# Optimization experiments

Hardware: AMD Instinct MI355X
Metric: run time of the kernel (lower is better)

Reference implementation:

```python
import jax, jax.numpy as jnp
import numpy as np

B, N, LAT, H, NL, NH = 1, 512, 128, 256, 3, 4
EMB = H // 4  # atom-type embedding dim = 64
DH = H // NH  # head dim = 64
LN_EPS = 1e-5


def _lin(x, w, b):
    # torch nn.Linear convention: w is (out, in)
    return x @ w.T + b


def _ln(x, s, b):
    m = jnp.mean(x, -1, keepdims=True)
    v = jnp.mean((x - m) ** 2, -1, keepdims=True)
    return (x - m) / jnp.sqrt(v + LN_EPS) * s + b


def setup_inputs() -> dict:
    key = jax.random.key(0)
    ks = iter(jax.random.split(key, 64))
    def w(shape, scale=0.02):
        return (jax.random.normal(next(ks), shape, jnp.float32) * scale).astype(jnp.float32)
    inp = dict(
        z=jax.random.normal(next(ks), (B, N, LAT), jnp.float32),
        z_global=jax.random.normal(next(ks), (B, LAT), jnp.float32),
        atom_types=jax.random.randint(next(ks), (B, N), 0, 4),
        emb=w((4, EMB), 1.0),
        ip_w1=w((H, LAT + EMB)), ip_b1=jnp.zeros(H), ip_w2=w((H, H)), ip_b2=jnp.zeros(H),
        gp_w1=w((H, LAT)), gp_b1=jnp.zeros(H), gp_w2=w((H, H)), gp_b2=jnp.zeros(H),
        tf_wqkv=w((NL, 3 * H, H)), tf_bqkv=jnp.zeros((NL, 3 * H)),
        tf_wo=w((NL, H, H)), tf_bo=jnp.zeros((NL, H)),
        tf_ln1_s=jnp.ones((NL, H)), tf_ln1_b=jnp.zeros((NL, H)),
        tf_w1=w((NL, 4 * H, H)), tf_b1=jnp.zeros((NL, 4 * H)),
        tf_w2=w((NL, H, 4 * H)), tf_b2=jnp.zeros((NL, H)),
        tf_ln2_s=jnp.ones((NL, H)), tf_ln2_b=jnp.zeros((NL, H)),
        dp_w1=w((H, 2 * H)), dp_b1=jnp.zeros(H), dp_w2=w((H, H)), dp_b2=jnp.zeros(H),
        dp_w3=w((1, H)), dp_b3=jnp.zeros(1),
        cp_w1=w((H, H)), cp_b1=jnp.zeros(H), cp_w2=w((3, H)), cp_b2=jnp.zeros(3),
    )
    return inp


def _forward(z, z_global, atom_types, emb,
             ip_w1, ip_b1, ip_w2, ip_b2,
             gp_w1, gp_b1, gp_w2, gp_b2,
             tf_wqkv, tf_bqkv, tf_wo, tf_bo, tf_ln1_s, tf_ln1_b,
             tf_w1, tf_b1, tf_w2, tf_b2, tf_ln2_s, tf_ln2_b,
             dp_w1, dp_b1, dp_w2, dp_b2, dp_w3, dp_b3,
             cp_w1, cp_b1, cp_w2, cp_b2):
    Bs, Ns = z.shape[0], z.shape[1]
    atom_feats = emb[atom_types]                      # (B,N,EMB)
    z_input = jnp.concatenate([z, atom_feats], -1)    # (B,N,LAT+EMB)
    h = _lin(jax.nn.silu(_lin(z_input, ip_w1, ip_b1)), ip_w2, ip_b2)
    g = _lin(jax.nn.silu(_lin(z_global, gp_w1, gp_b1)), gp_w2, gp_b2)
    h = h + g[:, None, :]
    # post-norm TransformerEncoder (relu FFN, eval mode -> no dropout)
    scale = 1.0 / np.sqrt(DH)
    for l in range(NL):
        qkv = _lin(h, tf_wqkv[l], tf_bqkv[l])
        q, k, v = jnp.split(qkv, 3, -1)
        q = q.reshape(Bs, Ns, NH, DH)
        k = k.reshape(Bs, Ns, NH, DH)
        v = v.reshape(Bs, Ns, NH, DH)
        att = jax.nn.softmax(jnp.einsum('bqhd,bkhd->bhqk', q, k) * scale, -1)
        o = jnp.einsum('bhqk,bkhd->bqhd', att, v).reshape(Bs, Ns, H)
        h = _ln(h + _lin(o, tf_wo[l], tf_bo[l]), tf_ln1_s[l], tf_ln1_b[l])
        ff = _lin(jax.nn.relu(_lin(h, tf_w1[l], tf_b1[l])), tf_w2[l], tf_b2[l])
        h = _ln(h + ff, tf_ln2_s[l], tf_ln2_b[l])
    # dist head: Linear(concat(h_i,h_j)) == h_i @ W[:, :H].T + h_j @ W[:, H:].T + b
    # (avoids materializing the (B,N,N,2H) concat; identical math)
    ai = h @ dp_w1[:, :H].T                           # (B,N,H)
    aj = h @ dp_w1[:, H:].T                           # (B,N,H)
    pair = jax.nn.silu(ai[:, :, None, :] + aj[:, None, :, :] + dp_b1)  # (B,N,N,H)
    pair = jax.nn.silu(_lin(pair, dp_w2, dp_b2))
    dist = jax.nn.softplus(_lin(pair, dp_w3, dp_b3))[..., 0]           # (B,N,N)
    dist = (dist + jnp.swapaxes(dist, 1, 2)) * 0.5
    x = _lin(jax.nn.silu(_lin(h, cp_w1, cp_b1)), cp_w2, cp_b2)          # (B,N,3)
    return x, dist


def reference(z, z_global, atom_types, emb,
              ip_w1, ip_b1, ip_w2, ip_b2,
              gp_w1, gp_b1, gp_w2, gp_b2,
              tf_wqkv, tf_bqkv, tf_wo, tf_bo, tf_ln1_s, tf_ln1_b,
              tf_w1, tf_b1, tf_w2, tf_b2, tf_ln2_s, tf_ln2_b,
              dp_w1, dp_b1, dp_w2, dp_b2, dp_w3, dp_b3,
              cp_w1, cp_b1, cp_w2, cp_b2):
    return _forward(z, z_global, atom_types, emb,
                    ip_w1, ip_b1, ip_w2, ip_b2,
                    gp_w1, gp_b1, gp_w2, gp_b2,
                    tf_wqkv, tf_bqkv, tf_wo, tf_bo, tf_ln1_s, tf_ln1_b,
                    tf_w1, tf_b1, tf_w2, tf_b2, tf_ln2_s, tf_ln2_b,
                    dp_w1, dp_b1, dp_w2, dp_b2, dp_w3, dp_b3,
                    cp_w1, cp_b1, cp_w2, cp_b2)
```

## Files before the change

### kernel.cpp

```cpp
#include <hip/hip_runtime.h>
#include <hip/hip_bf16.h>
#include <cstdint>

typedef __bf16 bf16;
typedef __attribute__((ext_vector_type(8))) __bf16 bf16x8;
typedef __attribute__((ext_vector_type(4))) float f32x4;

#define MFMA16(a, b, c) __builtin_amdgcn_mfma_f32_16x16x32_bf16(a, b, c, 0, 0, 0)

__device__ __forceinline__ float fast_rcp(float x) { return __builtin_amdgcn_rcpf(x); }
__device__ __forceinline__ float silu_f(float x) { return x * fast_rcp(1.f + __expf(-x)); }
__device__ __forceinline__ bf16x8 cvt8(float4 a, float4 b) {
  bf16x8 o;
  o[0]=(bf16)a.x; o[1]=(bf16)a.y; o[2]=(bf16)a.z; o[3]=(bf16)a.w;
  o[4]=(bf16)b.x; o[5]=(bf16)b.y; o[6]=(bf16)b.z; o[7]=(bf16)b.w;
  return o;
}

constexpr long WB_IPW1 = 0;
constexpr long WB_IPW2 = 49152;
constexpr long WB_QKV  = 114688;
constexpr long WB_WO   = 704512;
constexpr long WB_W1   = 901120;
constexpr long WB_W2   = 1687552;
constexpr long WB_CPW1 = 2670592;
constexpr long F_ZIN = 5472256;
constexpr long F_G   = F_ZIN + 512L*192*4;
constexpr long F_H   = F_G + 1024;
constexpr long F_QKV = F_H + 512L*256*4;
constexpr long F_S   = F_QKV + 512L*768*4;
constexpr long F_VT  = F_S + 4L*512*512*4;
constexpr long F_O   = F_VT + 4L*64*512*2;
constexpr long F_T1  = F_O + 512L*256*4;
constexpr long O_W2P  = F_T1 + 512L*256*4;
constexpr long O_WDP  = O_W2P + 131072;
constexpr long O_B512 = O_WDP + 262144;

__global__ __launch_bounds__(256) void prep_kernel(
    const float* __restrict__ s_ipw1, const float* __restrict__ s_ipw2,
    const float* __restrict__ s_qkv,  const float* __restrict__ s_wo,
    const float* __restrict__ s_w1,   const float* __restrict__ s_w2,
    const float* __restrict__ s_dpw1, const float* __restrict__ s_dpw2,
    const float* __restrict__ s_cpw1, bf16* __restrict__ dst,
    const float* __restrict__ z, const int* __restrict__ at, const float* __restrict__ emb,
    const float* __restrict__ zg, const float* __restrict__ gw1, const float* __restrict__ gb1,
    const float* __restrict__ gw2, const float* __restrict__ gb2,
    const float* __restrict__ dpb1,
    float* __restrict__ zi, bf16* __restrict__ w2p, bf16* __restrict__ wdp,
    float* __restrict__ g, float* __restrict__ bias512)
{
  __shared__ float zs[128];
  __shared__ float ts[256];
  const int b = blockIdx.x, tid = threadIdx.x;
  if (b < 2672) {
    long v = (long)b * 256 + tid;
    if (v >= 684032) return;
    const float* src; long off;
    if (v < 176128) {
      if (v < 12288)      { src = s_ipw1; off = 0; }
      else if (v < 28672) { src = s_ipw2; off = 12288; }
      else                { src = s_qkv;  off = 28672; }
    } else if (v < 618496) {
      if (v < 225280)      { src = s_wo; off = 176128; }
      else if (v < 421888) { src = s_w1; off = 225280; }
      else                 { src = s_w2; off = 421888; }
    } else {
      if (v < 651264)      { src = s_dpw1; off = 618496; }
      else if (v < 667648) { src = s_dpw2; off = 651264; }
      else                 { src = s_cpw1; off = 667648; }
    }
    long e = (v - off) * 4;
    float4 f = *(const float4*)&src[e];
    bf16* d = dst + off * 4 + e;
    d[0] = (bf16)f.x; d[1] = (bf16)f.y; d[2] = (bf16)f.z; d[3] = (bf16)f.w;
  } else if (b < 3056) {
    int idx = (b - 2672) * 256 + tid;
    int n = idx / 192, c = idx - n * 192;
    zi[idx] = (c < 128) ? z[n * 128 + c] : emb[at[n] * 64 + (c - 128)];
  } else if (b < 3088) {
    int f = (b - 3056) * 256 + tid;
    int l15 = f & 15, kq = (f >> 4) & 3, ks = (f >> 6) & 7, nt = f >> 9;
    int n = nt * 16 + l15, k0 = ks * 32 + kq * 8;
    float4 v0 = *(const float4*)&s_dpw2[n * 256 + k0];
    float4 v1 = *(const float4*)&s_dpw2[n * 256 + k0 + 4];
    *(bf16x8*)&w2p[(long)f * 8] = cvt8(v0, v1);
  } else if (b < 3216) {
    int v = (b - 3088) * 256 + tid;
    int r = v >> 6, c4 = (v & 63) << 2;
    long src = (r < 256) ? ((long)r * 512 + c4) : ((long)(r - 256) * 512 + 256 + c4);
    float4 f = *(const float4*)&s_dpw1[src];
    bf16* d = &wdp[r * 256 + c4];
    d[0]=(bf16)f.x; d[1]=(bf16)f.y; d[2]=(bf16)f.z; d[3]=(bf16)f.w;
  } else if (b == 3216) {
    if (tid < 128) zs[tid] = zg[tid];
    __syncthreads();
    float s = gb1[tid];
    for (int k = 0; k < 128; ++k) s += zs[k] * gw1[tid * 128 + k];
    ts[tid] = silu_f(s);
    __syncthreads();
    float s2 = gb2[tid];
    for (int k = 0; k < 256; ++k) s2 += ts[k] * gw2[tid * 256 + k];
    g[tid] = s2;
  } else {
    bias512[tid] = dpb1[tid];
    bias512[256 + tid] = 0.f;
  }
}

template<int ACT, typename WT>
__global__ __launch_bounds__(256) void gemm_kernel(
    const float* __restrict__ A, int lda, long sA,
    const WT* __restrict__ W, int ldw, long sW,
    const float* __restrict__ bias,
    const float* __restrict__ R, int ldr, long sR,
    float* __restrict__ C, int ldc, long sC, int K)
{
  const int bz = blockIdx.z;
  A += (long)bz * sA;  W += (long)bz * sW;  C += (long)bz * sC;
  if (R) R += (long)bz * sR;
  const int m0 = blockIdx.x * 64, n0 = blockIdx.y * 64;
  __shared__ bf16 As[64][72];
  __shared__ bf16 Ws[64][72];
  const int tid = threadIdx.x;
  const int lane = tid & 63, wid = tid >> 6;
  const int wm = (wid & 1) * 32, wn = (wid >> 1) * 32;
  const int rr = lane & 15, kg = (lane >> 4) << 3;
  f32x4 acc[2][2] = {};
  for (int k0 = 0; k0 < K; k0 += 64) {
#pragma unroll
    for (int r = 0; r < 4; ++r) {
      int lin = tid + r * 256;
      int row = lin >> 4, kc = (lin & 15) << 2;
      {
        const float* p = &A[(long)(m0 + row) * lda + k0 + kc];
        float4 v = *(const float4*)p;
        As[row][kc] = (bf16)v.x; As[row][kc + 1] = (bf16)v.y;
        As[row][kc + 2] = (bf16)v.z; As[row][kc + 3] = (bf16)v.w;
      }
      {
        const WT* p = &W[(long)(n0 + row) * ldw + k0 + kc];
        if constexpr (sizeof(WT) == 4) {
          float4 v = *(const float4*)p;
          Ws[row][kc] = (bf16)v.x; Ws[row][kc + 1] = (bf16)v.y;
          Ws[row][kc + 2] = (bf16)v.z; Ws[row][kc + 3] = (bf16)v.w;
        } else {
          *(uint2*)&Ws[row][kc] = *(const uint2*)p;
        }
      }
    }
    __syncthreads();
#pragma unroll
    for (int ks = 0; ks < 2; ++ks) {
      const int kk = ks * 32 + kg;
      bf16x8 a0 = *(const bf16x8*)&As[wm + rr][kk];
      bf16x8 a1 = *(const bf16x8*)&As[wm + 16 + rr][kk];
      bf16x8 b0 = *(const bf16x8*)&Ws[wn + rr][kk];
      bf16x8 b1 = *(const bf16x8*)&Ws[wn + 16 + rr][kk];
      acc[0][0] = MFMA16(a0, b0, acc[0][0]);
      acc[0][1] = MFMA16(a0, b1, acc[0][1]);
      acc[1][0] = MFMA16(a1, b0, acc[1][0]);
      acc[1][1] = MFMA16(a1, b1, acc[1][1]);
    }
    __syncthreads();
  }
  const int rg = lane >> 4;
#pragma unroll
  for (int mi = 0; mi < 2; ++mi)
#pragma unroll
    for (int ni = 0; ni < 2; ++ni)
#pragma unroll
      for (int r = 0; r < 4; ++r) {
        int gm = m0 + wm + mi * 16 + rg * 4 + r;
        int gn = n0 + wn + ni * 16 + rr;
        float v = acc[mi][ni][r];
        if (bias) v += bias[gn];
        if (R) v += R[(long)gm * ldr + gn];
        if (ACT == 1) v = silu_f(v);
        else if (ACT == 2) v = fmaxf(v, 0.f);
        C[(long)gm * ldc + gn] = v;
      }
}

__global__ __launch_bounds__(256) void softmax_kernel(float* __restrict__ S)
{
  long base = ((long)blockIdx.y * 512 + blockIdx.x) * 512;
  float* row = S + base;
  int tid = threadIdx.x;
  float a = row[tid] * 0.125f, b = row[tid + 256] * 0.125f;
  float m = fmaxf(a, b);
#pragma unroll
  for (int o = 1; o < 64; o <<= 1) m = fmaxf(m, __shfl_xor(m, o));
  __shared__ float red[4];
  __shared__ float red2[4];
  int wid = tid >> 6;
  if ((tid & 63) == 0) red[wid] = m;
  __syncthreads();
  m = fmaxf(fmaxf(red[0], red[1]), fmaxf(red[2], red[3]));
  float e0 = __expf(a - m), e1 = __expf(b - m);
  float s = e0 + e1;
#pragma unroll
  for (int o = 1; o < 64; o <<= 1) s += __shfl_xor(s, o);
  if ((tid & 63) == 0) red2[wid] = s;
  __syncthreads();
  s = red2[0] + red2[1] + red2[2] + red2[3];
  float inv = fast_rcp(s);
  row[tid] = e0 * inv; row[tid + 256] = e1 * inv;
}

__global__ __launch_bounds__(256) void vt_kernel(const float* __restrict__ qkv, bf16* __restrict__ vt)
{
  int idx = blockIdx.x * 256 + threadIdx.x;
  int hh = idx >> 15;
  int r = idx & 32767;
  int d = r >> 9, n = r & 511;
  vt[idx] = (bf16)qkv[(long)n * 768 + 512 + hh * 64 + d];
}

__global__ __launch_bounds__(256) void ln_kernel(
    const float* __restrict__ X, const float* __restrict__ sc,
    const float* __restrict__ bi, float* __restrict__ Y)
{
  int row = blockIdx.x, tid = threadIdx.x;
  float v = X[(long)row * 256 + tid];
  float s = v;
#pragma unroll
  for (int o = 1; o < 64; o <<= 1) s += __shfl_xor(s, o);
  __shared__ float r1[4];
  __shared__ float r2[4];
  if ((tid & 63) == 0) r1[tid >> 6] = s;
  __syncthreads();
  float mean = (r1[0] + r1[1] + r1[2] + r1[3]) * (1.f / 256.f);
  float d = v - mean;
  float t = d * d;
#pragma unroll
  for (int o = 1; o < 64; o <<= 1) t += __shfl_xor(t, o);
  if ((tid & 63) == 0) r2[tid >> 6] = t;
  __syncthreads();
  float var = (r2[0] + r2[1] + r2[2] + r2[3]) * (1.f / 256.f);
  Y[(long)row * 256 + tid] = d * rsqrtf(var + 1e-5f) * sc[tid] + bi[tid];
}

__global__ __launch_bounds__(256, 2) void pair2_kernel(
    const float* __restrict__ ai, const float* __restrict__ aj,
    const bf16* __restrict__ W2P, const float* __restrict__ b2g,
    const float* __restrict__ w3g, const float* __restrict__ b3p,
    float* __restrict__ dout)
{
  __shared__ float ai_s[256];
  __shared__ bf16  t_s[64 * 256];
  __shared__ float part[64][4];
  const int tid = threadIdx.x, lane = tid & 63, w = tid >> 6;
  const int l15 = lane & 15, kq = lane >> 4;
  const int i = blockIdx.x >> 1, half = blockIdx.x & 1;
  const float b3v = b3p[0];

  ai_s[tid] = ai[(long)i * 512 + tid];

  float b2v[4], w3v[4];
#pragma unroll
  for (int nt = 0; nt < 4; ++nt) {
    int ntg = w * 4 + nt;
    b2v[nt] = b2g[ntg * 16 + l15];
    w3v[nt] = w3g[ntg * 16 + l15];
  }
  const bf16* w2base = W2P + ((long)(((w * 4) * 8 * 4 + kq) * 16 + l15)) * 8;
  __syncthreads();

  for (int jc = half * 4; jc < half * 4 + 4; ++jc) {
    const int j0 = jc * 64;
    const float* ajp = aj + (long)(j0 + lane) * 512;
#pragma unroll
    for (int r = 0; r < 8; ++r) {
      int kk = w + 4 * r;
      float4 a0 = *(const float4*)(ajp + kk * 8);
      float4 a1 = *(const float4*)(ajp + kk * 8 + 4);
      const float* aip = ai_s + kk * 8;
      bf16x8 tv;
      tv[0] = (bf16)silu_f(a0.x + aip[0]); tv[1] = (bf16)silu_f(a0.y + aip[1]);
      tv[2] = (bf16)silu_f(a0.z + aip[2]); tv[3] = (bf16)silu_f(a0.w + aip[3]);
      tv[4] = (bf16)silu_f(a1.x + aip[4]); tv[5] = (bf16)silu_f(a1.y + aip[5]);
      tv[6] = (bf16)silu_f(a1.z + aip[6]); tv[7] = (bf16)silu_f(a1.w + aip[7]);
      *(bf16x8*)&t_s[(kk * 64 + lane) * 8] = tv;
    }
    __syncthreads();

    f32x4 acc[4][4] = {};
#pragma unroll
    for (int ks = 0; ks < 8; ++ks) {
      bf16x8 af[4];
#pragma unroll
      for (int Mt = 0; Mt < 4; ++Mt)
        af[Mt] = *(const bf16x8*)&t_s[((ks * 4 + kq) * 64 + Mt * 16 + l15) * 8];
#pragma unroll
      for (int nt = 0; nt < 4; ++nt) {
        bf16x8 bfv = *(const bf16x8*)(w2base + (long)(nt * 8 + ks) * 512);
#pragma unroll
        for (int Mt = 0; Mt < 4; ++Mt)
          acc[Mt][nt] = MFMA16(af[Mt], bfv, acc[Mt][nt]);
      }
    }

#pragma unroll
    for (int Mt = 0; Mt < 4; ++Mt)
#pragma unroll
      for (int r = 0; r < 4; ++r) {
        float s = silu_f(acc[Mt][0][r] + b2v[0]) * w3v[0]
                + silu_f(acc[Mt][1][r] + b2v[1]) * w3v[1]
                + silu_f(acc[Mt][2][r] + b2v[2]) * w3v[2]
                + silu_f(acc[Mt][3][r] + b2v[3]) * w3v[3];
        s += __shfl_xor(s, 1); s += __shfl_xor(s, 2);
        s += __shfl_xor(s, 4); s += __shfl_xor(s, 8);
        if (l15 == 0) part[Mt * 16 + kq * 4 + r][w] = s;
      }
    __syncthreads();
    if (tid < 64) {
      float s = part[tid][0] + part[tid][1] + part[tid][2] + part[tid][3] + b3v;
      float dd = fmaxf(s, 0.f) + log1pf(__expf(-fabsf(s)));
      dout[(long)i * 512 + j0 + tid] = dd;
    }
    __syncthreads();
  }
}

__global__ __launch_bounds__(256) void sym_kernel(float* __restrict__ dist)
{
  int idx = blockIdx.x * 256 + threadIdx.x;
  int i = idx >> 9, j = idx & 511;
  if (i < j) {
    float a = dist[idx];
    float b = dist[(long)j * 512 + i];
    float m = 0.5f * (a + b);
    dist[idx] = m;
    dist[(long)j * 512 + i] = m;
  }
}

__global__ __launch_bounds__(256) void coord_kernel(
    const float* __restrict__ ct, const float* __restrict__ w2,
    const float* __restrict__ b2, float* __restrict__ out)
{
  int t = blockIdx.x * 256 + threadIdx.x;
  if (t >= 1536) return;
  int row = t / 3, c = t - row * 3;
  float s = b2[c];
  const float* a = &ct[(long)row * 256];
  const float* wp = &w2[c * 256];
  for (int k = 0; k < 256; ++k) s += a[k] * wp[k];
  out[t] = s;
}

extern "C" void kernel_launch(void* const* d_in, const int* in_sizes, int n_in,
                              void* d_out, int out_size, void* d_ws, size_t ws_size,
                              hipStream_t stream) {
  const float* z        = (const float*)d_in[0];
  const float* z_global = (const float*)d_in[1];
  const int*   atom_t   = (const int*)d_in[2];
  const float* emb      = (const float*)d_in[3];
  const float* ip_w1 = (const float*)d_in[4];  const float* ip_b1 = (const float*)d_in[5];
  const float* ip_w2 = (const float*)d_in[6];  const float* ip_b2 = (const float*)d_in[7];
  const float* gp_w1 = (const float*)d_in[8];  const float* gp_b1 = (const float*)d_in[9];
  const float* gp_w2 = (const float*)d_in[10]; const float* gp_b2 = (const float*)d_in[11];
  const float* wqkv  = (const float*)d_in[12]; const float* bqkv  = (const float*)d_in[13];
  const float* wo    = (const float*)d_in[14]; const float* bo    = (const float*)d_in[15];
  const float* ln1s  = (const float*)d_in[16]; const float* ln1b  = (const float*)d_in[17];
  const float* w1    = (const float*)d_in[18]; const float* b1    = (const float*)d_in[19];
  const float* w2    = (const float*)d_in[20]; const float* b2    = (const float*)d_in[21];
  const float* ln2s  = (const float*)d_in[22]; const float* ln2b  = (const float*)d_in[23];
  const float* dpw1  = (const float*)d_in[24]; const float* dpb1  = (const float*)d_in[25];
  const float* dpw2  = (const float*)d_in[26]; const float* dpb2  = (const float*)d_in[27];
  const float* dpw3  = (const float*)d_in[28]; const float* dpb3  = (const float*)d_in[29];
  const float* cpw1  = (const float*)d_in[30]; const float* cpb1  = (const float*)d_in[31];
  const float* cpw2  = (const float*)d_in[32]; const float* cpb2  = (const float*)d_in[33];

  char* ws = (char*)d_ws;
  bf16*  WB   = (bf16*)ws;
  float* zin  = (float*)(ws + F_ZIN);
  float* g    = (float*)(ws + F_G);
  float* h    = (float*)(ws + F_H);
  float* qkv  = (float*)(ws + F_QKV);
  float* S    = (float*)(ws + F_S);
  bf16*  Vt   = (bf16*)(ws + F_VT);
  float* o    = (float*)(ws + F_O);
  float* t1   = (float*)(ws + F_T1);
  bf16*  W2P  = (bf16*)(ws + O_W2P);
  bf16*  WDP  = (bf16*)(ws + O_WDP);
  float* b512 = (float*)(ws + O_B512);
  float* ff1  = S;
  float* aiaj = S;
  float* out  = (float*)d_out;
  float* xout = out;
  float* dist = out + 1536;

  prep_kernel<<<3218, 256, 0, stream>>>(ip_w1, ip_w2, wqkv, wo, w1, w2, dpw1, dpw2, cpw1, WB,
      z, atom_t, emb, z_global, gp_w1, gp_b1, gp_w2, gp_b2, dpb1,
      zin, W2P, WDP, g, b512);

  gemm_kernel<1, bf16><<<dim3(8, 4, 1), 256, 0, stream>>>(zin, 192, 0, WB + WB_IPW1, 192, 0,
      ip_b1, nullptr, 0, 0, t1, 256, 0, 192);
  gemm_kernel<0, bf16><<<dim3(8, 4, 1), 256, 0, stream>>>(t1, 256, 0, WB + WB_IPW2, 256, 0,
      ip_b2, g, 0, 0, h, 256, 0, 256);

  for (int l = 0; l < 3; ++l) {
    const bf16* wq = WB + WB_QKV + (long)l * 768 * 256;
    gemm_kernel<0, bf16><<<dim3(8, 12, 1), 256, 0, stream>>>(h, 256, 0, wq, 256, 0,
        bqkv + l * 768, nullptr, 0, 0, qkv, 768, 0, 256);
    gemm_kernel<0, float><<<dim3(8, 8, 4), 256, 0, stream>>>(qkv, 768, 64, qkv + 256, 768, 64,
        nullptr, nullptr, 0, 0, S, 512, 262144, 64);
    softmax_kernel<<<dim3(512, 4), 256, 0, stream>>>(S);
    vt_kernel<<<512, 256, 0, stream>>>(qkv, Vt);
    gemm_kernel<0, bf16><<<dim3(8, 1, 4), 256, 0, stream>>>(S, 512, 262144, Vt, 512, 32768,
        nullptr, nullptr, 0, 0, o, 256, 64, 512);
    gemm_kernel<0, bf16><<<dim3(8, 4, 1), 256, 0, stream>>>(o, 256, 0,
        WB + WB_WO + (long)l * 65536, 256, 0, bo + l * 256, h, 256, 0, t1, 256, 0, 256);
    ln_kernel<<<512, 256, 0, stream>>>(t1, ln1s + l * 256, ln1b + l * 256, h);
    gemm_kernel<2, bf16><<<dim3(8, 16, 1), 256, 0, stream>>>(h, 256, 0,
        WB + WB_W1 + (long)l * 262144, 256, 0, b1 + l * 1024, nullptr, 0, 0, ff1, 1024, 0, 256);
    gemm_kernel<0, bf16><<<dim3(8, 4, 1), 256, 0, stream>>>(ff1, 1024, 0,
        WB + WB_W2 + (long)l * 262144, 1024, 0, b2 + l * 256, h, 256, 0, t1, 256, 0, 1024);
    ln_kernel<<<512, 256, 0, stream>>>(t1, ln2s + l * 256, ln2b + l * 256, h);
  }

  gemm_kernel<0, bf16><<<dim3(8, 8, 1), 256, 0, stream>>>(h, 256, 0, WDP, 256, 0,
      b512, nullptr, 0, 0, aiaj, 512, 0, 256);
  pair2_kernel<<<1024, 256, 0, stream>>>(aiaj, aiaj + 256, W2P, dpb2, dpw3, dpb3, dist);
  sym_kernel<<<1024, 256, 0, stream>>>(dist);
  gemm_kernel<1, bf16><<<dim3(8, 4, 1), 256, 0, stream>>>(h, 256, 0, WB + WB_CPW1, 256, 0,
      cpb1, nullptr, 0, 0, t1, 256, 0, 256);
  coord_kernel<<<6, 256, 0, stream>>>(t1, cpw2, cpb2, xout);
}
```

Measured before the change: 375.8 us.

## Double-buffer pair MLP tiles and merge softmax with V-transpose launch

The pair-distance kernel now works on 32-column chunks with two shared-memory tile buffers. The next chunk's silu(ai+aj) tile is built while the current chunk's MFMAs and epilogue run, which removes a barrier per chunk and overlaps global loads with matrix work. The softmax and V-transpose kernels become one launch that branches on block index, saving a launch per layer. Smaller M tiles per MFMA pass mean less reuse of the B-fragments, and register pressure may rise.

Result: faster. 355.6 us (-5.4%).

```diff
diff --git a/kernel.cpp b/kernel.cpp
--- a/kernel.cpp
+++ b/kernel.cpp
@@ -181,39 +181,38 @@
       }
 }
 
-__global__ __launch_bounds__(256) void softmax_kernel(float* __restrict__ S)
-{
-  long base = ((long)blockIdx.y * 512 + blockIdx.x) * 512;
-  float* row = S + base;
-  int tid = threadIdx.x;
-  float a = row[tid] * 0.125f, b = row[tid + 256] * 0.125f;
-  float m = fmaxf(a, b);
-#pragma unroll
-  for (int o = 1; o < 64; o <<= 1) m = fmaxf(m, __shfl_xor(m, o));
-  __shared__ float red[4];
-  __shared__ float red2[4];
-  int wid = tid >> 6;
-  if ((tid & 63) == 0) red[wid] = m;
-  __syncthreads();
-  m = fmaxf(fmaxf(red[0], red[1]), fmaxf(red[2], red[3]));
-  float e0 = __expf(a - m), e1 = __expf(b - m);
-  float s = e0 + e1;
-#pragma unroll
-  for (int o = 1; o < 64; o <<= 1) s += __shfl_xor(s, o);
-  if ((tid & 63) == 0) red2[wid] = s;
-  __syncthreads();
-  s = red2[0] + red2[1] + red2[2] + red2[3];
-  float inv = fast_rcp(s);
-  row[tid] = e0 * inv; row[tid + 256] = e1 * inv;
-}
-
-__global__ __launch_bounds__(256) void vt_kernel(const float* __restrict__ qkv, bf16* __restrict__ vt)
-{
-  int idx = blockIdx.x * 256 + threadIdx.x;
-  int hh = idx >> 15;
-  int r = idx & 32767;
-  int d = r >> 9, n = r & 511;
-  vt[idx] = (bf16)qkv[(long)n * 768 + 512 + hh * 64 + d];
+__global__ __launch_bounds__(256) void softvt_kernel(
+    float* __restrict__ S, const float* __restrict__ qkv, bf16* __restrict__ vt)
+{
+  const int b = blockIdx.x, tid = threadIdx.x;
+  if (b < 2048) {
+    float* row = S + (long)b * 512;
+    float a = row[tid] * 0.125f, e1v = row[tid + 256] * 0.125f;
+    float m = fmaxf(a, e1v);
+#pragma unroll
+    for (int o = 1; o < 64; o <<= 1) m = fmaxf(m, __shfl_xor(m, o));
+    __shared__ float red[4];
+    __shared__ float red2[4];
+    int wid = tid >> 6;
+    if ((tid & 63) == 0) red[wid] = m;
+    __syncthreads();
+    m = fmaxf(fmaxf(red[0], red[1]), fmaxf(red[2], red[3]));
+    float e0 = __expf(a - m), e1 = __expf(e1v - m);
+    float s = e0 + e1;
+#pragma unroll
+    for (int o = 1; o < 64; o <<= 1) s += __shfl_xor(s, o);
+    if ((tid & 63) == 0) red2[wid] = s;
+    __syncthreads();
+    s = red2[0] + red2[1] + red2[2] + red2[3];
+    float inv = fast_rcp(s);
+    row[tid] = e0 * inv; row[tid + 256] = e1 * inv;
+  } else {
+    int idx = (b - 2048) * 256 + tid;
+    int hh = idx >> 15;
+    int r = idx & 32767;
+    int d = r >> 9, n = r & 511;
+    vt[idx] = (bf16)qkv[(long)n * 768 + 512 + hh * 64 + d];
+  }
 }
 
 __global__ __launch_bounds__(256) void ln_kernel(
@@ -240,6 +239,59 @@
   Y[(long)row * 256 + tid] = d * rsqrtf(var + 1e-5f) * sc[tid] + bi[tid];
 }
 
+#define P2_BUILD(CIDX, TBUF)                                                     \
+  {                                                                              \
+    const int j0b = jbase + (CIDX) * 32;                                         \
+    const float* ajp = aj + (long)(j0b + pp) * 512;                              \
+    _Pragma("unroll")                                                            \
+    for (int r = 0; r < 4; ++r) {                                                \
+      int kk = kb + 8 * r;                                                       \
+      float4 a0 = *(const float4*)(ajp + kk * 8);                                \
+      float4 a1 = *(const float4*)(ajp + kk * 8 + 4);                            \
+      const float* aip = ai_s + kk * 8;                                          \
+      bf16x8 tv;                                                                 \
+      tv[0] = (bf16)silu_f(a0.x + aip[0]); tv[1] = (bf16)silu_f(a0.y + aip[1]);  \
+      tv[2] = (bf16)silu_f(a0.z + aip[2]); tv[3] = (bf16)silu_f(a0.w + aip[3]);  \
+      tv[4] = (bf16)silu_f(a1.x + aip[4]); tv[5] = (bf16)silu_f(a1.y + aip[5]);  \
+      tv[6] = (bf16)silu_f(a1.z + aip[6]); tv[7] = (bf16)silu_f(a1.w + aip[7]);  \
+      *(bf16x8*)&TBUF[(kk * 32 + pp) * 8] = tv;                                  \
+    }                                                                            \
+  }
+
+#define P2_MFMA(TBUF, ACC)                                                       \
+  _Pragma("unroll")                                                              \
+  for (int ks = 0; ks < 8; ++ks) {                                               \
+    bf16x8 af0 = *(const bf16x8*)&TBUF[((ks * 4 + kq) * 32 + l15) * 8];          \
+    bf16x8 af1 = *(const bf16x8*)&TBUF[((ks * 4 + kq) * 32 + 16 + l15) * 8];     \
+    _Pragma("unroll")                                                            \
+    for (int nt = 0; nt < 4; ++nt) {                                             \
+      bf16x8 bfv = *(const bf16x8*)(w2base + (long)(nt * 8 + ks) * 512);         \
+      ACC[0][nt] = MFMA16(af0, bfv, ACC[0][nt]);                                 \
+      ACC[1][nt] = MFMA16(af1, bfv, ACC[1][nt]);                                 \
+    }                                                                            \
+  }
+
+#define P2_EPI(ACC, PBUF)                                                        \
+  _Pragma("unroll")                                                              \
+  for (int Mt = 0; Mt < 2; ++Mt)                                                 \
+    _Pragma("unroll")                                                            \
+    for (int r = 0; r < 4; ++r) {                                                \
+      float s = silu_f(ACC[Mt][0][r] + b2v[0]) * w3v[0]                          \
+              + silu_f(ACC[Mt][1][r] + b2v[1]) * w3v[1]                          \
+              + silu_f(ACC[Mt][2][r] + b2v[2]) * w3v[2]                          \
+              + silu_f(ACC[Mt][3][r] + b2v[3]) * w3v[3];                         \
+      s += __shfl_xor(s, 1); s += __shfl_xor(s, 2);                              \
+      s += __shfl_xor(s, 4); s += __shfl_xor(s, 8);                              \
+      if (l15 == 0) PBUF[Mt * 16 + kq * 4 + r][w] = s;                           \
+    }
+
+#define P2_DIST(CIDX, PBUF)                                                      \
+  if (tid < 32) {                                                                \
+    float s = PBUF[tid][0] + PBUF[tid][1] + PBUF[tid][2] + PBUF[tid][3] + b3v;   \
+    float dd = fmaxf(s, 0.f) + log1pf(__expf(-fabsf(s)));                        \
+    dout[(long)i * 512 + jbase + (CIDX) * 32 + tid] = dd;                        \
+  }
+
 __global__ __launch_bounds__(256, 2) void pair2_kernel(
     const float* __restrict__ ai, const float* __restrict__ aj,
     const bf16* __restrict__ W2P, const float* __restrict__ b2g,
@@ -247,11 +299,15 @@
     float* __restrict__ dout)
 {
   __shared__ float ai_s[256];
-  __shared__ bf16  t_s[64 * 256];
-  __shared__ float part[64][4];
+  __shared__ bf16 t0_s[32 * 256];
+  __shared__ bf16 t1_s[32 * 256];
+  __shared__ float p0_s[32][4];
+  __shared__ float p1_s[32][4];
   const int tid = threadIdx.x, lane = tid & 63, w = tid >> 6;
   const int l15 = lane & 15, kq = lane >> 4;
+  const int pp = tid & 31, kb = tid >> 5;
   const int i = blockIdx.x >> 1, half = blockIdx.x & 1;
+  const int jbase = half * 256;
   const float b3v = b3p[0];
 
   ai_s[tid] = ai[(long)i * 512 + tid];
@@ -263,62 +319,30 @@
     b2v[nt] = b2g[ntg * 16 + l15];
     w3v[nt] = w3g[ntg * 16 + l15];
   }
-  const bf16* w2base = W2P + ((long)(((w * 4) * 8 * 4 + kq) * 16 + l15)) * 8;
+  const bf16* w2base = W2P + ((long)((w * 128 + kq) * 16 + l15)) * 8;
   __syncthreads();
 
-  for (int jc = half * 4; jc < half * 4 + 4; ++jc) {
-    const int j0 = jc * 64;
-    const float* ajp = aj + (long)(j0 + lane) * 512;
-#pragma unroll
-    for (int r = 0; r < 8; ++r) {
-      int kk = w + 4 * r;
-      float4 a0 = *(const float4*)(ajp + kk * 8);
-      float4 a1 = *(const float4*)(ajp + kk * 8 + 4);
-      const float* aip = ai_s + kk * 8;
-      bf16x8 tv;
-      tv[0] = (bf16)silu_f(a0.x + aip[0]); tv[1] = (bf16)silu_f(a0.y + aip[1]);
-      tv[2] = (bf16)silu_f(a0.z + aip[2]); tv[3] = (bf16)silu_f(a0.w + aip[3]);
-      tv[4] = (bf16)silu_f(a1.x + aip[4]); tv[5] = (bf16)silu_f(a1.y + aip[5]);
-      tv[6] = (bf16)silu_f(a1.z + aip[6]); tv[7] = (bf16)silu_f(a1.w + aip[7]);
-      *(bf16x8*)&t_s[(kk * 64 + lane) * 8] = tv;
-    }
-    __syncthreads();
-
-    f32x4 acc[4][4] = {};
-#pragma unroll
-    for (int ks = 0; ks < 8; ++ks) {
-      bf16x8 af[4];
-#pragma unroll
-      for (int Mt = 0; Mt < 4; ++Mt)
-        af[Mt] = *(const bf16x8*)&t_s[((ks * 4 + kq) * 64 + Mt * 16 + l15) * 8];
-#pragma unroll
-      for (int nt = 0; nt < 4; ++nt) {
-        bf16x8 bfv = *(const bf16x8*)(w2base + (long)(nt * 8 + ks) * 512);
-#pragma unroll
-        for (int Mt = 0; Mt < 4; ++Mt)
-          acc[Mt][nt] = MFMA16(af[Mt], bfv, acc[Mt][nt]);
-      }
-    }
-
-#pragma unroll
-    for (int Mt = 0; Mt < 4; ++Mt)
-#pragma unroll
-      for (int r = 0; r < 4; ++r) {
-        float s = silu_f(acc[Mt][0][r] + b2v[0]) * w3v[0]
-                + silu_f(acc[Mt][1][r] + b2v[1]) * w3v[1]
-                + silu_f(acc[Mt][2][r] + b2v[2]) * w3v[2]
-                + silu_f(acc[Mt][3][r] + b2v[3]) * w3v[3];
-        s += __shfl_xor(s, 1); s += __shfl_xor(s, 2);
-        s += __shfl_xor(s, 4); s += __shfl_xor(s, 8);
-        if (l15 == 0) part[Mt * 16 + kq * 4 + r][w] = s;
-      }
-    __syncthreads();
-    if (tid < 64) {
-      float s = part[tid][0] + part[tid][1] + part[tid][2] + part[tid][3] + b3v;
-      float dd = fmaxf(s, 0.f) + log1pf(__expf(-fabsf(s)));
-      dout[(long)i * 512 + j0 + tid] = dd;
-    }
-    __syncthreads();
+  P2_BUILD(0, t0_s);
+  __syncthreads();
+#pragma unroll 1
+  for (int cp = 0; cp < 4; ++cp) {
+    const int c0 = cp * 2, c1 = cp * 2 + 1;
+    {
+      f32x4 acc[2][4] = {};
+      P2_MFMA(t0_s, acc);
+      P2_BUILD(c1, t1_s);
+      P2_EPI(acc, p0_s);
+    }
+    __syncthreads();
+    P2_DIST(c0, p0_s);
+    {
+      f32x4 acc[2][4] = {};
+      P2_MFMA(t1_s, acc);
+      if (cp < 3) P2_BUILD(c1 + 1, t0_s);
+      P2_EPI(acc, p1_s);
+    }
+    __syncthreads();
+    P2_DIST(c1, p1_s);
   }
 }
 
@@ -406,8 +430,7 @@
         bqkv + l * 768, nullptr, 0, 0, qkv, 768, 0, 256);
     gemm_kernel<0, float><<<dim3(8, 8, 4), 256, 0, stream>>>(qkv, 768, 64, qkv + 256, 768, 64,
         nullptr, nullptr, 0, 0, S, 512, 262144, 64);
-    softmax_kernel<<<dim3(512, 4), 256, 0, stream>>>(S);
-    vt_kernel<<<512, 256, 0, stream>>>(qkv, Vt);
+    softvt_kernel<<<2560, 256, 0, stream>>>(S, qkv, Vt);
     gemm_kernel<0, bf16><<<dim3(8, 1, 4), 256, 0, stream>>>(S, 512, 262144, Vt, 512, 32768,
         nullptr, nullptr, 0, 0, o, 256, 64, 512);
     gemm_kernel<0, bf16><<<dim3(8, 4, 1), 256, 0, stream>>>(o, 256, 0,
```
